# Kernel optimization log

Measured on AMD Instinct MI355X. Metric: run time of the kernel, lower is better.

The kernel has to match this reference:

```python
import jax, jax.numpy as jnp
import numpy as np

# --- static hash-grid config (matches tcnn HashGrid in the torch module) ---
DIM = 3
N_LEVELS = 16
F = 2                      # n_features_per_level
LOG2_T = 19
T = 1 << LOG2_T            # hashmap size per level
BASE_RES = 16
TARGET_RES = 2048
PLS = float(np.exp2(np.log2(TARGET_RES / BASE_RES) / (N_LEVELS - 1)))  # per_level_scale
SCALES = [BASE_RES * PLS ** l for l in range(N_LEVELS)]
PRIMES = np.array([1, 2654435761, 805459861], dtype=np.uint32)
# 8 corner offsets of the unit cube, shape [8, 3]
OFFS = np.stack(np.meshgrid(*([np.arange(2)] * DIM), indexing='ij'), -1).reshape(-1, DIM).astype(np.float32)


def _hash(idx_u32):
    # idx_u32: [..., 3] uint32 -> [...] uint32 index into table of size T (power of 2)
    h = idx_u32[..., 0] * jnp.uint32(PRIMES[0])
    h = h ^ (idx_u32[..., 1] * jnp.uint32(PRIMES[1]))
    h = h ^ (idx_u32[..., 2] * jnp.uint32(PRIMES[2]))
    return h & jnp.uint32(T - 1)


def hashgrid_encode(x, table):
    # x: [N, 3] in [0,1); table: [L, T, F] fp32
    outs = []
    offs = jnp.asarray(OFFS)                      # [8, 3]
    for l in range(N_LEVELS):
        pos = x * jnp.float32(SCALES[l])          # [N, 3]
        base = jnp.floor(pos)
        frac = pos - base                         # [N, 3]
        corner = base[:, None, :] + offs[None]    # [N, 8, 3]
        idx = corner.astype(jnp.uint32)
        h = _hash(idx)                            # [N, 8]
        feat = table[l][h]                        # [N, 8, F] (gather)
        # trilinear weights: prod over dims of frac or (1-frac)
        w = jnp.prod(jnp.where(offs[None] > 0.5, frac[:, None, :], 1.0 - frac[:, None, :]), axis=-1)  # [N, 8]
        outs.append(jnp.sum(w[..., None] * feat, axis=1))  # [N, F]
    return jnp.concatenate(outs, axis=-1)         # [N, L*F] = [N, 32]


def setup_inputs() -> dict:
    key = jax.random.key(0)
    ks = jax.random.split(key, 8)
    N = 1048576
    dim_in = N_LEVELS * F          # 32
    hid = 16                       # (16+15)//16*16
    dout = 16                      # grid_output_dim
    x = jax.random.uniform(ks[0], (N, DIM), dtype=jnp.float32)
    table = jax.random.uniform(ks[1], (N_LEVELS, T, F), dtype=jnp.float32, minval=-1e-4, maxval=1e-4)
    def lin(k, fi, fo):
        b = 1.0 / np.sqrt(fi)
        return jax.random.uniform(k, (fo, fi), dtype=jnp.float32, minval=-b, maxval=b)
    W0 = lin(ks[2], dim_in, hid); b0 = jnp.zeros((hid,), jnp.float32)
    W1 = lin(ks[3], hid, hid);    b1 = jnp.zeros((hid,), jnp.float32)
    W2 = lin(ks[4], hid, dout);   b2 = jnp.zeros((dout,), jnp.float32)
    return {"x": x, "table": table, "W0": W0, "b0": b0, "W1": W1, "b1": b1, "W2": W2, "b2": b2}


def reference(x, table, W0, b0, W1, b1, W2, b2):
    h = hashgrid_encode(x, table)                 # [N, 32]
    h = jax.nn.relu(h @ W0.T + b0)
    h = jax.nn.relu(h @ W1.T + b1)
    return h @ W2.T + b2                          # [N, 16]
```

## Files before the change

### kernel.cpp

```cpp
#include <hip/hip_runtime.h>
#include <math.h>

#define NLV 16
#define LOG2_T 19
#define T_SIZE (1u << LOG2_T)
#define T_MASK (T_SIZE - 1u)
#define P2 2654435761u
#define P3 805459861u
#define NBUCK 32768

typedef float vf2 __attribute__((ext_vector_type(2)));
typedef float vf4 __attribute__((ext_vector_type(4)));

struct Scales { float s[NLV]; };

__device__ __forceinline__ unsigned mpart(unsigned v) {
    v = (v | (v << 8)) & 0x100Fu;
    v = (v | (v << 4)) & 0x10C3u;
    v = (v | (v << 2)) & 0x1249u;
    return v;
}
__device__ __forceinline__ unsigned mkey(float px, float py, float pz) {
    unsigned cx = (unsigned)(px * 32.f); cx = cx > 31u ? 31u : cx;
    unsigned cy = (unsigned)(py * 32.f); cy = cy > 31u ? 31u : cy;
    unsigned cz = (unsigned)(pz * 32.f); cz = cz > 31u ? 31u : cz;
    return mpart(cx) | (mpart(cy) << 1) | (mpart(cz) << 2);
}

__global__ __launch_bounds__(256) void zero_hist_kernel(unsigned* hist) {
    int i = blockIdx.x * 256 + threadIdx.x;
    if (i < NBUCK) hist[i] = 0u;
}

__global__ __launch_bounds__(256) void hist_kernel(
    const float* __restrict__ x, unsigned* __restrict__ hist, int N)
{
    int i = blockIdx.x * 256 + threadIdx.x;
    if (i >= N) return;
    const float px = x[3 * (size_t)i + 0];
    const float py = x[3 * (size_t)i + 1];
    const float pz = x[3 * (size_t)i + 2];
    atomicAdd(&hist[mkey(px, py, pz)], 1u);
}

__global__ __launch_bounds__(1024) void scan_kernel(unsigned* hist) {
    __shared__ unsigned tot[1024];
    const int t = threadIdx.x;
    const unsigned base = (unsigned)t * 32u;
    unsigned loc[32];
    unsigned s = 0;
    #pragma unroll
    for (int k = 0; k < 32; ++k) { loc[k] = s; s += hist[base + k]; }
    tot[t] = s;
    __syncthreads();
    for (int off = 1; off < 1024; off <<= 1) {
        unsigned u = (t >= off) ? tot[t - off] : 0u;
        __syncthreads();
        tot[t] += u;
        __syncthreads();
    }
    const unsigned excl = tot[t] - s;
    #pragma unroll
    for (int k = 0; k < 32; ++k) hist[base + k] = excl + loc[k];
}

__global__ __launch_bounds__(256) void scatter_kernel(
    const float* __restrict__ x, unsigned* __restrict__ cursor,
    vf4* __restrict__ xs, int* __restrict__ perm, int N)
{
    int i = blockIdx.x * 256 + threadIdx.x;
    if (i >= N) return;
    const float px = x[3 * (size_t)i + 0];
    const float py = x[3 * (size_t)i + 1];
    const float pz = x[3 * (size_t)i + 2];
    const unsigned key = mkey(px, py, pz);
    const unsigned pos = atomicAdd(&cursor[key], 1u);
    vf4 v; v[0] = px; v[1] = py; v[2] = pz; v[3] = 0.f;
    xs[pos] = v;
    perm[pos] = i;
}

__device__ __forceinline__ void enc_level(
    float px, float py, float pz, float s, const float* __restrict__ tl,
    float& f0, float& f1)
{
    const float fx = px * s, fy = py * s, fz = pz * s;
    const float bx = floorf(fx), by = floorf(fy), bz = floorf(fz);
    const float rx = fx - bx, ry = fy - by, rz = fz - bz;
    const unsigned ix0 = (unsigned)bx, iy0 = (unsigned)by, iz0 = (unsigned)bz;
    const unsigned hx0 = ix0,      hx1 = ix0 + 1u;
    const unsigned hy0 = iy0 * P2, hy1 = (iy0 + 1u) * P2;
    const unsigned hz0 = iz0 * P3, hz1 = (iz0 + 1u) * P3;
    const float wx0 = 1.f - rx, wy0 = 1.f - ry, wz0 = 1.f - rz;
    f0 = 0.f; f1 = 0.f;
    #pragma unroll
    for (int c = 0; c < 8; ++c) {
        unsigned h = ((c & 4) ? hx1 : hx0) ^ ((c & 2) ? hy1 : hy0) ^ ((c & 1) ? hz1 : hz0);
        h &= T_MASK;
        const vf2 f = *(const vf2*)(tl + 2u * (size_t)h);
        const float w = ((c & 4) ? rx : wx0) * ((c & 2) ? ry : wy0) * ((c & 1) ? rz : wz0);
        f0 += w * f[0];
        f1 += w * f[1];
    }
}

__global__ __launch_bounds__(256) void encode_coarse_kernel(
    const vf4* __restrict__ xs, const float* __restrict__ table,
    float* __restrict__ enc, int N, Scales sc)
{
    int i = blockIdx.x * 256 + threadIdx.x;
    if (i >= N) return;
    const vf4 p = xs[i];
    #pragma unroll
    for (int l = 0; l < 5; ++l) {
        float f0, f1;
        enc_level(p[0], p[1], p[2], sc.s[l], table + (size_t)l * T_SIZE * 2u, f0, f1);
        vf2 v; v[0] = f0; v[1] = f1;
        __builtin_nontemporal_store(v, (vf2*)(enc + ((size_t)l * N + i) * 2u));
    }
}

__global__ __launch_bounds__(256) void encode_one_kernel(
    const vf4* __restrict__ xs, const float* __restrict__ tl, float s,
    float* __restrict__ encl, int N)
{
    int i0 = blockIdx.x * 512 + threadIdx.x;
    int i1 = i0 + 256;
    if (i0 < N) {
        const vf4 p0 = xs[i0];
        const vf4 p1 = (i1 < N) ? xs[i1] : p0;
        float a0, a1, b0v, b1v;
        enc_level(p0[0], p0[1], p0[2], s, tl, a0, a1);
        enc_level(p1[0], p1[1], p1[2], s, tl, b0v, b1v);
        vf2 va; va[0] = a0; va[1] = a1;
        __builtin_nontemporal_store(va, (vf2*)(encl + (size_t)i0 * 2u));
        if (i1 < N) {
            vf2 vb; vb[0] = b0v; vb[1] = b1v;
            __builtin_nontemporal_store(vb, (vf2*)(encl + (size_t)i1 * 2u));
        }
    }
}

__global__ __launch_bounds__(256) void mlp_kernel(
    const float* __restrict__ enc, const int* __restrict__ perm,
    const float* __restrict__ W0, const float* __restrict__ b0,
    const float* __restrict__ W1, const float* __restrict__ b1,
    const float* __restrict__ W2, const float* __restrict__ b2,
    float* __restrict__ out, int N)
{
    __shared__ float st[256 * 17];
    const int base = blockIdx.x * 256;
    const int t = threadIdx.x;
    const int i = base + t;

    float o[16];
    if (i < N) {
        float e[32];
        #pragma unroll
        for (int l = 0; l < NLV; ++l) {
            vf2 v = *(const vf2*)(enc + ((size_t)l * N + i) * 2u);
            e[2 * l + 0] = v[0];
            e[2 * l + 1] = v[1];
        }
        float a0[16];
        #pragma unroll
        for (int j = 0; j < 16; ++j) {
            float s = b0[j];
            #pragma unroll
            for (int k = 0; k < 32; ++k) s += e[k] * W0[j * 32 + k];
            a0[j] = fmaxf(s, 0.f);
        }
        float a1[16];
        #pragma unroll
        for (int j = 0; j < 16; ++j) {
            float s = b1[j];
            #pragma unroll
            for (int k = 0; k < 16; ++k) s += a0[k] * W1[j * 16 + k];
            a1[j] = fmaxf(s, 0.f);
        }
        #pragma unroll
        for (int j = 0; j < 16; ++j) {
            float s = b2[j];
            #pragma unroll
            for (int k = 0; k < 16; ++k) s += a1[k] * W2[j * 16 + k];
            o[j] = s;
        }
    } else {
        #pragma unroll
        for (int j = 0; j < 16; ++j) o[j] = 0.f;
    }

    #pragma unroll
    for (int q = 0; q < 4; ++q) {
        vf4 v; v[0] = o[4*q]; v[1] = o[4*q+1]; v[2] = o[4*q+2]; v[3] = o[4*q+3];
        *(vf4*)&st[t * 17 + 4 * q] = v;
    }
    __syncthreads();

    const int c = t & 3;
    #pragma unroll
    for (int w = 0; w < 4; ++w) {
        const int p = (t >> 2) + w * 64;
        const int gi = base + p;
        if (gi < N) {
            const int dst = perm[gi];
            const vf4 v = *(const vf4*)&st[p * 17 + 4 * c];
            *(vf4*)(out + 16 * (size_t)dst + 4 * c) = v;
        }
    }
}

__global__ __launch_bounds__(256) void encode_coarse_unsorted_kernel(
    const float* __restrict__ x, const float* __restrict__ table,
    float* __restrict__ enc, int N, Scales sc)
{
    int i = blockIdx.x * 256 + threadIdx.x;
    if (i >= N) return;
    const float px = x[3 * (size_t)i + 0];
    const float py = x[3 * (size_t)i + 1];
    const float pz = x[3 * (size_t)i + 2];
    #pragma unroll
    for (int l = 0; l < 5; ++l) {
        float f0, f1;
        enc_level(px, py, pz, sc.s[l], table + (size_t)l * T_SIZE * 2u, f0, f1);
        vf2 v; v[0] = f0; v[1] = f1;
        __builtin_nontemporal_store(v, (vf2*)(enc + ((size_t)l * N + i) * 2u));
    }
}
__global__ __launch_bounds__(256) void encode_one_unsorted_kernel(
    const float* __restrict__ x, const float* __restrict__ tl, float s,
    float* __restrict__ encl, int N)
{
    int i = blockIdx.x * 256 + threadIdx.x;
    if (i >= N) return;
    const float px = x[3 * (size_t)i + 0];
    const float py = x[3 * (size_t)i + 1];
    const float pz = x[3 * (size_t)i + 2];
    float f0, f1;
    enc_level(px, py, pz, s, tl, f0, f1);
    vf2 v; v[0] = f0; v[1] = f1;
    __builtin_nontemporal_store(v, (vf2*)(encl + (size_t)i * 2u));
}
__global__ __launch_bounds__(256) void mlp_noperm_kernel(
    const float* __restrict__ enc,
    const float* __restrict__ W0, const float* __restrict__ b0,
    const float* __restrict__ W1, const float* __restrict__ b1,
    const float* __restrict__ W2, const float* __restrict__ b2,
    float* __restrict__ out, int N)
{
    int i = blockIdx.x * 256 + threadIdx.x;
    if (i >= N) return;
    float e[32];
    #pragma unroll
    for (int l = 0; l < NLV; ++l) {
        vf2 v = *(const vf2*)(enc + ((size_t)l * N + i) * 2u);
        e[2 * l + 0] = v[0];
        e[2 * l + 1] = v[1];
    }
    float a0[16];
    #pragma unroll
    for (int j = 0; j < 16; ++j) {
        float s = b0[j];
        #pragma unroll
        for (int k = 0; k < 32; ++k) s += e[k] * W0[j * 32 + k];
        a0[j] = fmaxf(s, 0.f);
    }
    float a1[16];
    #pragma unroll
    for (int j = 0; j < 16; ++j) {
        float s = b1[j];
        #pragma unroll
        for (int k = 0; k < 16; ++k) s += a0[k] * W1[j * 16 + k];
        a1[j] = fmaxf(s, 0.f);
    }
    #pragma unroll
    for (int j = 0; j < 16; ++j) {
        float s = b2[j];
        #pragma unroll
        for (int k = 0; k < 16; ++k) s += a1[k] * W2[j * 16 + k];
        out[16 * (size_t)i + j] = s;
    }
}
__global__ __launch_bounds__(256) void tcnn_fused_kernel(
    const float* __restrict__ x, const float* __restrict__ table,
    const float* __restrict__ W0, const float* __restrict__ b0,
    const float* __restrict__ W1, const float* __restrict__ b1,
    const float* __restrict__ W2, const float* __restrict__ b2,
    float* __restrict__ out, int N, Scales sc)
{
    int i = blockIdx.x * blockDim.x + threadIdx.x;
    if (i >= N) return;
    const float px = x[3 * (size_t)i + 0];
    const float py = x[3 * (size_t)i + 1];
    const float pz = x[3 * (size_t)i + 2];
    float e[32];
    #pragma unroll
    for (int l = 0; l < NLV; ++l) {
        float f0, f1;
        enc_level(px, py, pz, sc.s[l], table + (size_t)l * T_SIZE * 2u, f0, f1);
        e[2 * l] = f0; e[2 * l + 1] = f1;
    }
    float a0[16];
    #pragma unroll
    for (int j = 0; j < 16; ++j) {
        float s = b0[j];
        #pragma unroll
        for (int k = 0; k < 32; ++k) s += e[k] * W0[j * 32 + k];
        a0[j] = fmaxf(s, 0.f);
    }
    float a1[16];
    #pragma unroll
    for (int j = 0; j < 16; ++j) {
        float s = b1[j];
        #pragma unroll
        for (int k = 0; k < 16; ++k) s += a0[k] * W1[j * 16 + k];
        a1[j] = fmaxf(s, 0.f);
    }
    #pragma unroll
    for (int j = 0; j < 16; ++j) {
        float s = b2[j];
        #pragma unroll
        for (int k = 0; k < 16; ++k) s += a1[k] * W2[j * 16 + k];
        out[16 * (size_t)i + j] = s;
    }
}

extern "C" void kernel_launch(void* const* d_in, const int* in_sizes, int n_in,
                              void* d_out, int out_size, void* d_ws, size_t ws_size,
                              hipStream_t stream) {
    const float* x     = (const float*)d_in[0];
    const float* table = (const float*)d_in[1];
    const float* W0    = (const float*)d_in[2];
    const float* b0    = (const float*)d_in[3];
    const float* W1    = (const float*)d_in[4];
    const float* b1    = (const float*)d_in[5];
    const float* W2    = (const float*)d_in[6];
    const float* b2    = (const float*)d_in[7];
    float* out = (float*)d_out;

    const int N = in_sizes[0] / 3;

    Scales sc;
    const double pls = exp2(log2(2048.0 / 16.0) / 15.0);
    for (int l = 0; l < NLV; ++l) sc.s[l] = (float)(16.0 * pow(pls, (double)l));

    const int block = 256;
    const int grid = (N + block - 1) / block;

    const size_t encB  = (size_t)N * 2u * NLV * sizeof(float);
    const size_t xsB   = (size_t)N * sizeof(float) * 4u;
    const size_t permB = (size_t)N * sizeof(int);
    const size_t histB = (size_t)NBUCK * sizeof(unsigned);

    if (ws_size >= encB + xsB + permB + histB) {
        float*    enc  = (float*)d_ws;
        vf4*      xs   = (vf4*)((char*)d_ws + encB);
        int*      perm = (int*)((char*)d_ws + encB + xsB);
        unsigned* hist = (unsigned*)((char*)d_ws + encB + xsB + permB);

        zero_hist_kernel<<<(NBUCK + 255) / 256, block, 0, stream>>>(hist);
        hist_kernel<<<grid, block, 0, stream>>>(x, hist, N);
        scan_kernel<<<1, 1024, 0, stream>>>(hist);
        scatter_kernel<<<grid, block, 0, stream>>>(x, hist, xs, perm, N);

        encode_coarse_kernel<<<grid, block, 0, stream>>>(xs, table, enc, N, sc);
        const int grid2 = (N + 511) / 512;
        for (int l = 5; l < NLV; ++l) {
            encode_one_kernel<<<grid2, block, 0, stream>>>(
                xs, table + (size_t)l * T_SIZE * 2u, sc.s[l],
                enc + (size_t)l * (size_t)N * 2u, N);
        }
        mlp_kernel<<<grid, block, 0, stream>>>(enc, perm, W0, b0, W1, b1, W2, b2, out, N);
    } else if (ws_size >= encB) {
        float* enc = (float*)d_ws;
        encode_coarse_unsorted_kernel<<<grid, block, 0, stream>>>(x, table, enc, N, sc);
        for (int l = 5; l < NLV; ++l) {
            encode_one_unsorted_kernel<<<grid, block, 0, stream>>>(
                x, table + (size_t)l * T_SIZE * 2u, sc.s[l],
                enc + (size_t)l * (size_t)N * 2u, N);
        }
        mlp_noperm_kernel<<<grid, block, 0, stream>>>(enc, W0, b0, W1, b1, W2, b2, out, N);
    } else {
        tcnn_fused_kernel<<<grid, block, 0, stream>>>(x, table, W0, b0, W1, b1, W2, b2,
                                                      out, N, sc);
    }
}
```

Measured before the change: 545.8 us.

## Vectorize x loads, widen per-thread work, drop nontemporal stores in encode

Hist and scatter kernels now process four points per thread and read x with three aligned 16-byte loads, replacing scalar strided loads. encode_one handles four points per thread instead of two, and the encoding writes become plain stores rather than nontemporal ones, so enc may stay in cache for the MLP pass. The MLP kernel handles two points per thread with 16-byte enc loads and a larger shared staging buffer. The changes cut load instruction count and launched blocks, at the cost of higher register pressure and lower occupancy in the MLP.

```diff
diff --git a/kernel.cpp b/kernel.cpp
--- a/kernel.cpp
+++ b/kernel.cpp
@@ -35,12 +35,22 @@
 __global__ __launch_bounds__(256) void hist_kernel(
     const float* __restrict__ x, unsigned* __restrict__ hist, int N)
 {
-    int i = blockIdx.x * 256 + threadIdx.x;
-    if (i >= N) return;
-    const float px = x[3 * (size_t)i + 0];
-    const float py = x[3 * (size_t)i + 1];
-    const float pz = x[3 * (size_t)i + 2];
-    atomicAdd(&hist[mkey(px, py, pz)], 1u);
+    const int q = blockIdx.x * 256 + threadIdx.x;
+    const int i0 = q * 4;
+    if (i0 >= N) return;
+    if (i0 + 3 < N) {
+        const vf4 A = *(const vf4*)(x + 12 * (size_t)q);
+        const vf4 B = *(const vf4*)(x + 12 * (size_t)q + 4);
+        const vf4 C = *(const vf4*)(x + 12 * (size_t)q + 8);
+        const float px[4] = {A[0], A[3], B[2], C[1]};
+        const float py[4] = {A[1], B[0], B[3], C[2]};
+        const float pz[4] = {A[2], B[1], C[0], C[3]};
+        #pragma unroll
+        for (int k = 0; k < 4; ++k) atomicAdd(&hist[mkey(px[k], py[k], pz[k])], 1u);
+    } else {
+        for (int i = i0; i < N; ++i)
+            atomicAdd(&hist[mkey(x[3*(size_t)i], x[3*(size_t)i+1], x[3*(size_t)i+2])], 1u);
+    }
 }
 
 __global__ __launch_bounds__(1024) void scan_kernel(unsigned* hist) {
@@ -68,16 +78,34 @@
     const float* __restrict__ x, unsigned* __restrict__ cursor,
     vf4* __restrict__ xs, int* __restrict__ perm, int N)
 {
-    int i = blockIdx.x * 256 + threadIdx.x;
-    if (i >= N) return;
-    const float px = x[3 * (size_t)i + 0];
-    const float py = x[3 * (size_t)i + 1];
-    const float pz = x[3 * (size_t)i + 2];
-    const unsigned key = mkey(px, py, pz);
-    const unsigned pos = atomicAdd(&cursor[key], 1u);
-    vf4 v; v[0] = px; v[1] = py; v[2] = pz; v[3] = 0.f;
-    xs[pos] = v;
-    perm[pos] = i;
+    const int q = blockIdx.x * 256 + threadIdx.x;
+    const int i0 = q * 4;
+    if (i0 >= N) return;
+    if (i0 + 3 < N) {
+        const vf4 A = *(const vf4*)(x + 12 * (size_t)q);
+        const vf4 B = *(const vf4*)(x + 12 * (size_t)q + 4);
+        const vf4 C = *(const vf4*)(x + 12 * (size_t)q + 8);
+        const float px[4] = {A[0], A[3], B[2], C[1]};
+        const float py[4] = {A[1], B[0], B[3], C[2]};
+        const float pz[4] = {A[2], B[1], C[0], C[3]};
+        #pragma unroll
+        for (int k = 0; k < 4; ++k) {
+            const unsigned key = mkey(px[k], py[k], pz[k]);
+            const unsigned pos = atomicAdd(&cursor[key], 1u);
+            vf4 v; v[0] = px[k]; v[1] = py[k]; v[2] = pz[k]; v[3] = 0.f;
+            xs[pos] = v;
+            perm[pos] = i0 + k;
+        }
+    } else {
+        for (int i = i0; i < N; ++i) {
+            const float px = x[3*(size_t)i], py = x[3*(size_t)i+1], pz = x[3*(size_t)i+2];
+            const unsigned key = mkey(px, py, pz);
+            const unsigned pos = atomicAdd(&cursor[key], 1u);
+            vf4 v; v[0] = px; v[1] = py; v[2] = pz; v[3] = 0.f;
+            xs[pos] = v;
+            perm[pos] = i;
+        }
+    }
 }
 
 __device__ __forceinline__ void enc_level(
@@ -116,7 +144,7 @@
         float f0, f1;
         enc_level(p[0], p[1], p[2], sc.s[l], table + (size_t)l * T_SIZE * 2u, f0, f1);
         vf2 v; v[0] = f0; v[1] = f1;
-        __builtin_nontemporal_store(v, (vf2*)(enc + ((size_t)l * N + i) * 2u));
+        *(vf2*)(enc + ((size_t)l * N + i) * 2u) = v;
     }
 }
 
@@ -124,19 +152,16 @@
     const vf4* __restrict__ xs, const float* __restrict__ tl, float s,
     float* __restrict__ encl, int N)
 {
-    int i0 = blockIdx.x * 512 + threadIdx.x;
-    int i1 = i0 + 256;
-    if (i0 < N) {
-        const vf4 p0 = xs[i0];
-        const vf4 p1 = (i1 < N) ? xs[i1] : p0;
-        float a0, a1, b0v, b1v;
-        enc_level(p0[0], p0[1], p0[2], s, tl, a0, a1);
-        enc_level(p1[0], p1[1], p1[2], s, tl, b0v, b1v);
-        vf2 va; va[0] = a0; va[1] = a1;
-        __builtin_nontemporal_store(va, (vf2*)(encl + (size_t)i0 * 2u));
-        if (i1 < N) {
-            vf2 vb; vb[0] = b0v; vb[1] = b1v;
-            __builtin_nontemporal_store(vb, (vf2*)(encl + (size_t)i1 * 2u));
+    const int i0 = blockIdx.x * 1024 + threadIdx.x;
+    #pragma unroll
+    for (int k = 0; k < 4; ++k) {
+        const int i = i0 + k * 256;
+        if (i < N) {
+            const vf4 p = xs[i];
+            float f0, f1;
+            enc_level(p[0], p[1], p[2], s, tl, f0, f1);
+            vf2 v; v[0] = f0; v[1] = f1;
+            *(vf2*)(encl + (size_t)i * 2u) = v;
         }
     }
 }
@@ -148,58 +173,56 @@
     const float* __restrict__ W2, const float* __restrict__ b2,
     float* __restrict__ out, int N)
 {
-    __shared__ float st[256 * 17];
-    const int base = blockIdx.x * 256;
+    __shared__ float st[512 * 17];
+    const int base = blockIdx.x * 512;
     const int t = threadIdx.x;
-    const int i = base + t;
-
-    float o[16];
-    if (i < N) {
-        float e[32];
+    const int p0 = base + 2 * t;
+
+    if (p0 < N) {
+        float e[64];
         #pragma unroll
         for (int l = 0; l < NLV; ++l) {
-            vf2 v = *(const vf2*)(enc + ((size_t)l * N + i) * 2u);
-            e[2 * l + 0] = v[0];
-            e[2 * l + 1] = v[1];
-        }
-        float a0[16];
-        #pragma unroll
-        for (int j = 0; j < 16; ++j) {
-            float s = b0[j];
-            #pragma unroll
-            for (int k = 0; k < 32; ++k) s += e[k] * W0[j * 32 + k];
-            a0[j] = fmaxf(s, 0.f);
-        }
-        float a1[16];
-        #pragma unroll
-        for (int j = 0; j < 16; ++j) {
-            float s = b1[j];
-            #pragma unroll
-            for (int k = 0; k < 16; ++k) s += a0[k] * W1[j * 16 + k];
-            a1[j] = fmaxf(s, 0.f);
-        }
-        #pragma unroll
-        for (int j = 0; j < 16; ++j) {
-            float s = b2[j];
-            #pragma unroll
-            for (int k = 0; k < 16; ++k) s += a1[k] * W2[j * 16 + k];
-            o[j] = s;
-        }
-    } else {
-        #pragma unroll
-        for (int j = 0; j < 16; ++j) o[j] = 0.f;
-    }
-
-    #pragma unroll
-    for (int q = 0; q < 4; ++q) {
-        vf4 v; v[0] = o[4*q]; v[1] = o[4*q+1]; v[2] = o[4*q+2]; v[3] = o[4*q+3];
-        *(vf4*)&st[t * 17 + 4 * q] = v;
+            vf4 v = *(const vf4*)(enc + ((size_t)l * N + p0) * 2u);
+            e[4*l+0] = v[0]; e[4*l+1] = v[1]; e[4*l+2] = v[2]; e[4*l+3] = v[3];
+        }
+        #pragma unroll
+        for (int q = 0; q < 2; ++q) {
+            if (q == 0 || p0 + 1 < N) {
+                float a0[16];
+                #pragma unroll
+                for (int j = 0; j < 16; ++j) {
+                    float s = b0[j];
+                    #pragma unroll
+                    for (int l = 0; l < NLV; ++l) {
+                        s += e[4*l + 2*q + 0] * W0[j * 32 + 2*l + 0];
+                        s += e[4*l + 2*q + 1] * W0[j * 32 + 2*l + 1];
+                    }
+                    a0[j] = fmaxf(s, 0.f);
+                }
+                float a1[16];
+                #pragma unroll
+                for (int j = 0; j < 16; ++j) {
+                    float s = b1[j];
+                    #pragma unroll
+                    for (int k = 0; k < 16; ++k) s += a0[k] * W1[j * 16 + k];
+                    a1[j] = fmaxf(s, 0.f);
+                }
+                const int row = 2 * t + q;
+                #pragma unroll
+                for (int j = 0; j < 16; ++j) {
+                    float s = b2[j];
+                    #pragma unroll
+                    for (int k = 0; k < 16; ++k) s += a1[k] * W2[j * 16 + k];
+                    st[row * 17 + j] = s;
+                }
+            }
+        }
     }
     __syncthreads();
 
     const int c = t & 3;
     #pragma unroll
-    for (int w = 0; w < 4; ++w) {
+    for (int w = 0; w < 8; ++w) {
         const int p = (t >> 2) + w * 64;
         const int gi = base + p;
         if (gi < N) {
@@ -224,7 +247,7 @@
         float f0, f1;
         enc_level(px, py, pz, sc.s[l], table + (size_t)l * T_SIZE * 2u, f0, f1);
         vf2 v; v[0] = f0; v[1] = f1;
-        __builtin_nontemporal_store(v, (vf2*)(enc + ((size_t)l * N + i) * 2u));
+        *(vf2*)(enc + ((size_t)l * N + i) * 2u) = v;
     }
 }
 __global__ __launch_bounds__(256) void encode_one_unsorted_kernel(
@@ -239,7 +262,7 @@
     float f0, f1;
     enc_level(px, py, pz, s, tl, f0, f1);
     vf2 v; v[0] = f0; v[1] = f1;
-    __builtin_nontemporal_store(v, (vf2*)(encl + (size_t)i * 2u));
+    *(vf2*)(encl + (size_t)i * 2u) = v;
 }
 __global__ __launch_bounds__(256) void mlp_noperm_kernel(
     const float* __restrict__ enc,
@@ -358,19 +381,20 @@
         int*      perm = (int*)((char*)d_ws + encB + xsB);
         unsigned* hist = (unsigned*)((char*)d_ws + encB + xsB + permB);
 
+        const int gridQ = (N + 1023) / 1024;
         zero_hist_kernel<<<(NBUCK + 255) / 256, block, 0, stream>>>(hist);
-        hist_kernel<<<grid, block, 0, stream>>>(x, hist, N);
+        hist_kernel<<<gridQ, block, 0, stream>>>(x, hist, N);
         scan_kernel<<<1, 1024, 0, stream>>>(hist);
-        scatter_kernel<<<grid, block, 0, stream>>>(x, hist, xs, perm, N);
+        scatter_kernel<<<gridQ, block, 0, stream>>>(x, hist, xs, perm, N);
 
         encode_coarse_kernel<<<grid, block, 0, stream>>>(xs, table, enc, N, sc);
-        const int grid2 = (N + 511) / 512;
         for (int l = 5; l < NLV; ++l) {
-            encode_one_kernel<<<grid2, block, 0, stream>>>(
+            encode_one_kernel<<<gridQ, block, 0, stream>>>(
                 xs, table + (size_t)l * T_SIZE * 2u, sc.s[l],
                 enc + (size_t)l * (size_t)N * 2u, N);
         }
-        mlp_kernel<<<grid, block, 0, stream>>>(enc, perm, W0, b0, W1, b1, W2, b2, out, N);
+        const int gridM = (N + 511) / 512;
+        mlp_kernel<<<gridM, block, 0, stream>>>(enc, perm, W0, b0, W1, b1, W2, b2, out, N);
     } else if (ws_size >= encB) {
         float* enc = (float*)d_ws;
         encode_coarse_unsorted_kernel<<<grid, block, 0, stream>>>(x, table, enc, N, sc);
```

After: 533.1 us. 1.02x faster.
